# Kernel tuning notes

Hardware: AMD Instinct MI355X
Metric: run time of the kernel (lower is better)

## Reference

```python
import jax, jax.numpy as jnp
import numpy as np

DELTA_V = 0.5
DELTA_D = 1.5
LOSS_WEIGHT = 1.0


def setup_inputs() -> dict:
    key = jax.random.key(0)
    k1, k2, k3, k4 = jax.random.split(key, 4)
    B, D, H, W = 8, 4, 640, 640
    return {
        "emb": jax.random.normal(k1, (B, D, H, W), dtype=jnp.float32),
        "instance": jax.random.randint(k2, (B, H, W), 0, 33, dtype=jnp.int32),
        "kernel": jax.random.uniform(k3, (B, H, W), dtype=jnp.float32),
        "training_mask": jax.random.uniform(k4, (B, H, W), dtype=jnp.float32),
        "num_labels": 33,  # static: background label 0 + 32 instances, all present w.h.p.
    }


def _single(emb, instance, kernel, tmask, num_labels):
    # emb: [D,H,W]; instance: [H,W] int; kernel/tmask: [H,W] float
    D = emb.shape[0]
    tm = (tmask > 0.5).astype(instance.dtype)
    kn = (kernel > 0.5).astype(instance.dtype)
    inst2 = instance * tm                      # instance masked by training mask
    inst_k = (inst2 * kn).reshape(-1)          # kernel-restricted labels, [N]
    inst = inst2.reshape(-1)                   # [N]
    x = emb.reshape(D, -1).T                   # [N, D]
    ones = jnp.ones(x.shape[0], jnp.float32)

    # per-instance kernel means (scatter-mean), label 0 column forced to zero
    sums = jax.ops.segment_sum(x, inst_k, num_segments=num_labels)      # [K1, D]
    cnts = jax.ops.segment_sum(ones, inst_k, num_segments=num_labels)   # [K1]
    mean = sums / jnp.maximum(cnts, 1.0)[:, None]
    mean = mean.at[0].set(0.0)

    # aggregation term: per-pixel distance to its instance mean, segmented mean over labels 1..K
    diff = x - mean[inst]                                               # [N, D]
    dist = jnp.sqrt(jnp.sum(diff * diff, axis=1))
    val = jnp.log(jnp.maximum(dist - DELTA_V, 0.0) ** 2 + 1.0)
    cnt_i = jax.ops.segment_sum(ones, inst, num_segments=num_labels)
    agg = jax.ops.segment_sum(val, inst, num_segments=num_labels) / jnp.maximum(cnt_i, 1.0)
    l_agg = jnp.mean(agg[1:])

    # discrimination term: pairwise distances between instance means (exclude label 0 and diagonal)
    m = mean[1:]                                                        # [K, D]
    K = m.shape[0]
    pdiff = m[:, None, :] - m[None, :, :]
    pd = jnp.sqrt(jnp.sum(pdiff * pdiff, axis=-1) + jnp.eye(K))         # diag padded (masked below)
    vald = jnp.log(jnp.maximum(2.0 * DELTA_D - pd, 0.0) ** 2 + 1.0)
    off = 1.0 - jnp.eye(K)
    l_dis = jnp.sum(vald * off) / (K * (K - 1))

    # regularizer: mean over all num_labels columns; label-0 column contributes log(1)=0
    nrm1 = jnp.sqrt(jnp.sum(m * m, axis=1))
    l_reg = jnp.sum(jnp.log(nrm1 + 1.0)) / num_labels * 0.001

    return l_agg + l_dis + l_reg


def reference(emb, instance, kernel, training_mask, num_labels):
    f = lambda e, i, k, t: _single(e, i, k, t, num_labels)
    loss_batch = jax.vmap(f)(emb, instance, kernel, training_mask)
    return jnp.mean(LOSS_WEIGHT * loss_batch)
```

## Files before the change

### kernel.cpp

```cpp
#include <hip/hip_runtime.h>
#include <math.h>

#define HW    409600
#define HW4   102400
#define BATCH 8
#define NLAB  33
#define GXB1  100
#define NREP  8
#define RS    201
#define MEANS_OFF 0
#define AWS_OFF   1344
#define P2_OFF    3008
#define P1_OFF    4096
#define LABS_OFF_F 164096
#define NEED_SPLIT ((size_t)(P1_OFF + BATCH*GXB1*200) * 4)
#define NEED_LABS  ((size_t)LABS_OFF_F * 4 + (size_t)BATCH * HW4 * 4)

#if defined(__has_builtin) && __has_builtin(__builtin_amdgcn_sched_barrier)
#define SCHED_PIN() __builtin_amdgcn_sched_barrier(0)
#else
#define SCHED_PIN()
#endif

__global__ void init_ws(float* ws, float* out) {
    int t = threadIdx.x;
    for (int i = t; i < AWS_OFF + BATCH * 208 - 0; i += 256)
        if (i >= AWS_OFF) ws[i] = 0.f;
    if (t == 0) out[0] = 0.f;
}

__device__ __forceinline__ float getc(const float4& v, int e) {
    return (e == 0) ? v.x : (e == 1) ? v.y : (e == 2) ? v.z : v.w;
}
__device__ __forceinline__ float wave_sum(float v) {
    #pragma unroll
    for (int o = 32; o > 0; o >>= 1) v += __shfl_xor(v, o);
    return v;
}

struct Quad { int4 iv; float4 tv, kv, x0, x1, x2, x3; };

__device__ __forceinline__ void loadQ(Quad& q, const int4* inst4, const float4* tm4,
                                      const float4* kern4, const float4* emb4, int g) {
    q.iv = inst4[g];
    q.tv = tm4[g];
    q.kv = kern4[g];
    q.x0 = emb4[g];
    q.x1 = emb4[g + HW4];
    q.x2 = emb4[g + 2 * HW4];
    q.x3 = emb4[g + 3 * HW4];
}

__device__ __forceinline__ void acc1(int l, bool k,
                                     float x0, float x1, float x2, float x3,
                                     float* mb) {
    if (l) {
        float* bb = mb + l * 6;
        atomicAdd(bb + 5, 1.f);
        if (k) {
            atomicAdd(bb + 0, x0);
            atomicAdd(bb + 1, x1);
            atomicAdd(bb + 2, x2);
            atomicAdd(bb + 3, x3);
            atomicAdd(bb + 4, 1.f);
        }
    }
}

__device__ __forceinline__ void procQ(const Quad& q, float* mb,
                                      unsigned* labs, size_t labidx) {
    int l0 = (q.tv.x > 0.5f) ? q.iv.x : 0;
    int l1 = (q.tv.y > 0.5f) ? q.iv.y : 0;
    int l2 = (q.tv.z > 0.5f) ? q.iv.z : 0;
    int l3 = (q.tv.w > 0.5f) ? q.iv.w : 0;
    if (labs)
        labs[labidx] = (unsigned)l0 | ((unsigned)l1 << 8) |
                       ((unsigned)l2 << 16) | ((unsigned)l3 << 24);
    acc1(l0, q.kv.x > 0.5f, q.x0.x, q.x1.x, q.x2.x, q.x3.x, mb);
    acc1(l1, q.kv.y > 0.5f, q.x0.y, q.x1.y, q.x2.y, q.x3.y, mb);
    acc1(l2, q.kv.z > 0.5f, q.x0.z, q.x1.z, q.x2.z, q.x3.z, mb);
    acc1(l3, q.kv.w > 0.5f, q.x0.w, q.x1.w, q.x2.w, q.x3.w, mb);
}

template<bool SPLIT>
__global__ __launch_bounds__(256, 4) void pass1(const float* __restrict__ emb,
                                                const int*   __restrict__ inst,
                                                const float* __restrict__ kern,
                                                const float* __restrict__ tmask,
                                                float*       __restrict__ ws,
                                                unsigned*    __restrict__ labs) {
    __shared__ float bins[NREP][RS];
    const int t = threadIdx.x, bx = blockIdx.x, b = blockIdx.y;
    float* mb = bins[(t >> 3) & (NREP - 1)];

    const size_t  base  = (size_t)b * HW;
    const float4* emb4  = (const float4*)(emb + base * 4);
    const int4*   inst4 = (const int4*)(inst + base);
    const float4* kern4 = (const float4*)(kern + base);
    const float4* tm4   = (const float4*)(tmask + base);
    const int q0 = bx * 1024 + t;
    const size_t lb = (size_t)b * HW4;

    Quad c0, c1;
    loadQ(c0, inst4, tm4, kern4, emb4, q0);
    loadQ(c1, inst4, tm4, kern4, emb4, q0 + 256);
    SCHED_PIN();

    for (int i = t; i < NREP * RS; i += 256) (&bins[0][0])[i] = 0.f;
    __syncthreads();

    procQ(c0, mb, labs, lb + q0);
    loadQ(c0, inst4, tm4, kern4, emb4, q0 + 512);
    SCHED_PIN();
    procQ(c1, mb, labs, lb + q0 + 256);
    loadQ(c1, inst4, tm4, kern4, emb4, q0 + 768);
    SCHED_PIN();
    procQ(c0, mb, labs, lb + q0 + 512);
    procQ(c1, mb, labs, lb + q0 + 768);
    __syncthreads();

    if (t < NLAB * 6) {
        float v = 0.f;
        #pragma unroll
        for (int r = 0; r < NREP; ++r) v += bins[r][t];
        if (SPLIT) {
            ws[P1_OFF + ((size_t)b * GXB1 + bx) * 200 + t] = v;
        } else {
            if (v != 0.f) atomicAdd(ws + AWS_OFF + b * 208 + t, v);
        }
    }
}

template<bool SPLIT>
__global__ __launch_bounds__(256) void reduce_means(float* __restrict__ ws) {
    __shared__ float raw[200];
    const int t = threadIdx.x, b = blockIdx.x;
    if (t < NLAB * 6) {
        float s = 0.f;
        if (SPLIT) {
            const float* p = ws + P1_OFF + (size_t)b * GXB1 * 200;
            for (int bx = 0; bx < GXB1; ++bx) s += p[bx * 200 + t];
        } else {
            s = ws[AWS_OFF + b * 208 + t];
        }
        raw[t] = s;
    }
    __syncthreads();
    float* mm = ws + MEANS_OFF + b * 168;
    if (t < NLAB) {
        float cntk = raw[t * 6 + 4], cnti = raw[t * 6 + 5];
        float inv = 1.f / fmaxf(cntk, 1.f);
        float z = (t == 0) ? 0.f : 1.f;
        mm[t * 4 + 0] = z * raw[t * 6 + 0] * inv;
        mm[t * 4 + 1] = z * raw[t * 6 + 1] * inv;
        mm[t * 4 + 2] = z * raw[t * 6 + 2] * inv;
        mm[t * 4 + 3] = z * raw[t * 6 + 3] * inv;
        mm[132 + t]   = 1.f / fmaxf(cnti, 1.f);
    }
}

struct Quad2 { unsigned pk; int4 iv; float4 tv, x0, x1, x2, x3; };

template<bool USE_LABS>
__device__ __forceinline__ void loadQ2(Quad2& q, const unsigned* labs, size_t lb,
                                       const int4* inst4, const float4* tm4,
                                       const float4* emb4, int g) {
    if (USE_LABS) {
        q.pk = labs[lb + g];
    } else {
        q.iv = inst4[g];
        q.tv = tm4[g];
    }
    q.x0 = emb4[g];
    q.x1 = emb4[g + HW4];
    q.x2 = emb4[g + 2 * HW4];
    q.x3 = emb4[g + 3 * HW4];
}

template<bool USE_LABS>
__device__ __forceinline__ float procQ2(const Quad2& q, const float4* means4,
                                        const float* invci) {
    unsigned pk;
    if (USE_LABS) {
        pk = q.pk;
    } else {
        pk = (unsigned)((q.tv.x > 0.5f) ? q.iv.x : 0)        |
             ((unsigned)((q.tv.y > 0.5f) ? q.iv.y : 0) << 8) |
             ((unsigned)((q.tv.z > 0.5f) ? q.iv.z : 0) << 16)|
             ((unsigned)((q.tv.w > 0.5f) ? q.iv.w : 0) << 24);
    }
    float acc = 0.f;
    #pragma unroll
    for (int e = 0; e < 4; ++e) {
        int l = (pk >> (8 * e)) & 255;
        if (l) {
            float4 m = means4[l];
            float d0 = getc(q.x0, e) - m.x, d1 = getc(q.x1, e) - m.y;
            float d2 = getc(q.x2, e) - m.z, d3 = getc(q.x3, e) - m.w;
            float dist = sqrtf(d0 * d0 + d1 * d1 + d2 * d2 + d3 * d3);
            float u = fmaxf(dist - 0.5f, 0.f);
            acc += __logf(u * u + 1.f) * invci[l];
        }
    }
    return acc;
}

template<bool USE_LABS>
__global__ __launch_bounds__(256, 4) void pass2(const float* __restrict__ emb,
                                                const int*   __restrict__ inst,
                                                const float* __restrict__ tmask,
                                                float*       __restrict__ ws,
                                                const unsigned* __restrict__ labs) {
    __shared__ float4 means4[NLAB];
    __shared__ float  invci[NLAB];
    __shared__ float  red[4];
    const int t = threadIdx.x, bx = blockIdx.x, b = blockIdx.y;

    const size_t  base  = (size_t)b * HW;
    const float4* emb4  = (const float4*)(emb + base * 4);
    const int4*   inst4 = (const int4*)(inst + base);
    const float4* tm4   = (const float4*)(tmask + base);
    const int q0 = bx * 1024 + t;
    const size_t lb = (size_t)b * HW4;

    Quad2 c0, c1;
    loadQ2<USE_LABS>(c0, labs, lb, inst4, tm4, emb4, q0);
    loadQ2<USE_LABS>(c1, labs, lb, inst4, tm4, emb4, q0 + 256);
    SCHED_PIN();

    const float* mm = ws + MEANS_OFF + b * 168;
    if (t < NLAB) {
        means4[t] = ((const float4*)mm)[t];
        invci[t]  = mm[132 + t];
    }
    __syncthreads();

    float acc = procQ2<USE_LABS>(c0, means4, invci);
    loadQ2<USE_LABS>(c0, labs, lb, inst4, tm4, emb4, q0 + 512);
    SCHED_PIN();
    acc += procQ2<USE_LABS>(c1, means4, invci);
    loadQ2<USE_LABS>(c1, labs, lb, inst4, tm4, emb4, q0 + 768);
    SCHED_PIN();
    acc += procQ2<USE_LABS>(c0, means4, invci);
    acc += procQ2<USE_LABS>(c1, means4, invci);

    acc = wave_sum(acc);
    if ((t & 63) == 0) red[t >> 6] = acc;
    __syncthreads();
    if (t == 0)
        ws[P2_OFF + b * 128 + bx] = red[0] + red[1] + red[2] + red[3];
}

__global__ __launch_bounds__(256) void final_kernel(const float* __restrict__ ws,
                                                    float* __restrict__ out) {
    __shared__ float4 means4[NLAB];
    __shared__ float  red[4];
    const int t = threadIdx.x, b = blockIdx.x;
    const float* mm = ws + MEANS_OFF + b * 168;
    if (t < NLAB) means4[t] = ((const float4*)mm)[t];
    __syncthreads();

    float part = (t < GXB1) ? ws[P2_OFF + b * 128 + t] * (1.f / 32.f) : 0.f;
    float disp = 0.f;
    for (int p = t; p < 1024; p += 256) {
        int i = p >> 5, j = p & 31;
        if (i != j) {
            float4 mi = means4[i + 1], mj = means4[j + 1];
            float d0 = mi.x - mj.x, d1 = mi.y - mj.y;
            float d2 = mi.z - mj.z, d3 = mi.w - mj.w;
            float pd = sqrtf(d0 * d0 + d1 * d1 + d2 * d2 + d3 * d3);
            float u = fmaxf(3.0f - pd, 0.f);
            disp += __logf(u * u + 1.f);
        }
    }
    disp *= 1.f / 992.f;
    float regp = 0.f;
    if (t >= 1 && t < NLAB) {
        float4 m = means4[t];
        float n2 = m.x * m.x + m.y * m.y + m.z * m.z + m.w * m.w;
        regp = __logf(sqrtf(n2) + 1.f) * (0.001f / 33.f);
    }

    float v = wave_sum(part + disp + regp);
    if ((t & 63) == 0) red[t >> 6] = v;
    __syncthreads();
    if (t == 0)
        atomicAdd(out, (red[0] + red[1] + red[2] + red[3]) * (1.f / BATCH));
}

extern "C" void kernel_launch(void* const* d_in, const int* in_sizes, int n_in,
                              void* d_out, int out_size, void* d_ws, size_t ws_size,
                              hipStream_t stream) {
    const float* emb   = (const float*)d_in[0];
    const int*   inst  = (const int*)  d_in[1];
    const float* kern  = (const float*)d_in[2];
    const float* tmask = (const float*)d_in[3];
    float* ws  = (float*)d_ws;
    float* out = (float*)d_out;

    const bool split    = ws_size >= NEED_SPLIT;
    const bool use_labs = ws_size >= NEED_LABS;
    unsigned* labs = use_labs ? (unsigned*)(ws + LABS_OFF_F) : nullptr;

    init_ws<<<1, 256, 0, stream>>>(ws, out);
    dim3 grid(GXB1, BATCH);
    if (split) pass1<true ><<<grid, 256, 0, stream>>>(emb, inst, kern, tmask, ws, labs);
    else       pass1<false><<<grid, 256, 0, stream>>>(emb, inst, kern, tmask, ws, labs);
    if (split) reduce_means<true ><<<BATCH, 256, 0, stream>>>(ws);
    else       reduce_means<false><<<BATCH, 256, 0, stream>>>(ws);
    if (use_labs) pass2<true ><<<grid, 256, 0, stream>>>(emb, inst, tmask, ws, labs);
    else          pass2<false><<<grid, 256, 0, stream>>>(emb, inst, tmask, ws, nullptr);
    final_kernel<<<BATCH, 256, 0, stream>>>(ws, out);
}
```

Baseline: 156.7 us.

## Double grid size, drop init kernel, single-block final reduction

Halves the work per block in pass1 and pass2 (512 quads instead of 1024, grid 200x8) and raises the occupancy hint to 8 blocks per CU. Removes the init launch when the split path is used, and makes final_kernel a single block that loops over the batch and writes the output directly instead of using an atomic. The aim is more parallelism across the GPU plus fewer launches and atomics. In exchange the per-block partials double, and each block has less load-ahead to hide latency.

```diff
diff --git a/kernel.cpp b/kernel.cpp
--- a/kernel.cpp
+++ b/kernel.cpp
@@ -5,15 +5,15 @@
 #define HW4   102400
 #define BATCH 8
 #define NLAB  33
-#define GXB1  100
+#define GXB   200
 #define NREP  8
 #define RS    201
 #define MEANS_OFF 0
-#define AWS_OFF   1344
-#define P2_OFF    3008
-#define P1_OFF    4096
-#define LABS_OFF_F 164096
-#define NEED_SPLIT ((size_t)(P1_OFF + BATCH*GXB1*200) * 4)
+#define P2_OFF    2048
+#define AWS_OFF   4096
+#define P1_OFF    8192
+#define LABS_OFF_F (P1_OFF + BATCH*GXB*200)
+#define NEED_SPLIT ((size_t)LABS_OFF_F * 4)
 #define NEED_LABS  ((size_t)LABS_OFF_F * 4 + (size_t)BATCH * HW4 * 4)
 
 #if defined(__has_builtin) && __has_builtin(__builtin_amdgcn_sched_barrier)
@@ -22,11 +22,9 @@
 #define SCHED_PIN()
 #endif
 
-__global__ void init_ws(float* ws, float* out) {
-    int t = threadIdx.x;
-    for (int i = t; i < AWS_OFF + BATCH * 208 - 0; i += 256)
-        if (i >= AWS_OFF) ws[i] = 0.f;
-    if (t == 0) out[0] = 0.f;
+__global__ void init_aws(float* ws) {
+    int i = blockIdx.x * 256 + threadIdx.x;
+    if (i < BATCH * 208) ws[AWS_OFF + i] = 0.f;
 }
 
 __device__ __forceinline__ float getc(const float4& v, int e) {
@@ -83,7 +81,7 @@
 }
 
 template<bool SPLIT>
-__global__ __launch_bounds__(256, 4) void pass1(const float* __restrict__ emb,
+__global__ __launch_bounds__(256, 8) void pass1(const float* __restrict__ emb,
                                                 const int*   __restrict__ inst,
                                                 const float* __restrict__ kern,
                                                 const float* __restrict__ tmask,
@@ -98,25 +96,19 @@
     const int4*   inst4 = (const int4*)(inst + base);
     const float4* kern4 = (const float4*)(kern + base);
     const float4* tm4   = (const float4*)(tmask + base);
-    const int q0 = bx * 1024 + t;
+    const int q0 = bx * 512 + t;
     const size_t lb = (size_t)b * HW4;
 
-    Quad c0, c1;
-    loadQ(c0, inst4, tm4, kern4, emb4, q0);
-    loadQ(c1, inst4, tm4, kern4, emb4, q0 + 256);
+    for (int i = t; i < NREP * RS; i += 256) (&bins[0][0])[i] = 0.f;
+    __syncthreads();
+
+    Quad q;
+    loadQ(q, inst4, tm4, kern4, emb4, q0);
     SCHED_PIN();
-
-    for (int i = t; i < NREP * RS; i += 256) (&bins[0][0])[i] = 0.f;
-    __syncthreads();
-
-    procQ(c0, mb, labs, lb + q0);
-    loadQ(c0, inst4, tm4, kern4, emb4, q0 + 512);
+    procQ(q, mb, labs, lb + q0);
+    loadQ(q, inst4, tm4, kern4, emb4, q0 + 256);
     SCHED_PIN();
-    procQ(c1, mb, labs, lb + q0 + 256);
-    loadQ(c1, inst4, tm4, kern4, emb4, q0 + 768);
-    SCHED_PIN();
-    procQ(c0, mb, labs, lb + q0 + 512);
-    procQ(c1, mb, labs, lb + q0 + 768);
+    procQ(q, mb, labs, lb + q0 + 256);
     __syncthreads();
 
     if (t < NLAB * 6) {
@@ -124,7 +116,7 @@
         #pragma unroll
         for (int r = 0; r < NREP; ++r) v += bins[r][t];
         if (SPLIT) {
-            ws[P1_OFF + ((size_t)b * GXB1 + bx) * 200 + t] = v;
+            ws[P1_OFF + ((size_t)b * GXB + bx) * 200 + t] = v;
         } else {
             if (v != 0.f) atomicAdd(ws + AWS_OFF + b * 208 + t, v);
         }
@@ -138,8 +130,15 @@
     if (t < NLAB * 6) {
         float s = 0.f;
         if (SPLIT) {
-            const float* p = ws + P1_OFF + (size_t)b * GXB1 * 200;
-            for (int bx = 0; bx < GXB1; ++bx) s += p[bx * 200 + t];
+            const float* p = ws + P1_OFF + (size_t)b * GXB * 200 + t;
+            float s0 = 0.f, s1 = 0.f, s2 = 0.f, s3 = 0.f;
+            for (int bx = 0; bx < GXB; bx += 4) {
+                s0 += p[(bx + 0) * 200];
+                s1 += p[(bx + 1) * 200];
+                s2 += p[(bx + 2) * 200];
+                s3 += p[(bx + 3) * 200];
+            }
+            s = (s0 + s1) + (s2 + s3);
         } else {
             s = ws[AWS_OFF + b * 208 + t];
         }
@@ -206,7 +205,7 @@
 }
 
 template<bool USE_LABS>
-__global__ __launch_bounds__(256, 4) void pass2(const float* __restrict__ emb,
+__global__ __launch_bounds__(256, 8) void pass2(const float* __restrict__ emb,
                                                 const int*   __restrict__ inst,
                                                 const float* __restrict__ tmask,
                                                 float*       __restrict__ ws,
@@ -220,12 +219,11 @@
     const float4* emb4  = (const float4*)(emb + base * 4);
     const int4*   inst4 = (const int4*)(inst + base);
     const float4* tm4   = (const float4*)(tmask + base);
-    const int q0 = bx * 1024 + t;
+    const int q0 = bx * 512 + t;
     const size_t lb = (size_t)b * HW4;
 
-    Quad2 c0, c1;
-    loadQ2<USE_LABS>(c0, labs, lb, inst4, tm4, emb4, q0);
-    loadQ2<USE_LABS>(c1, labs, lb, inst4, tm4, emb4, q0 + 256);
+    Quad2 q;
+    loadQ2<USE_LABS>(q, labs, lb, inst4, tm4, emb4, q0);
     SCHED_PIN();
 
     const float* mm = ws + MEANS_OFF + b * 168;
@@ -235,57 +233,56 @@
     }
     __syncthreads();
 
-    float acc = procQ2<USE_LABS>(c0, means4, invci);
-    loadQ2<USE_LABS>(c0, labs, lb, inst4, tm4, emb4, q0 + 512);
+    float acc = procQ2<USE_LABS>(q, means4, invci);
+    loadQ2<USE_LABS>(q, labs, lb, inst4, tm4, emb4, q0 + 256);
     SCHED_PIN();
-    acc += procQ2<USE_LABS>(c1, means4, invci);
-    loadQ2<USE_LABS>(c1, labs, lb, inst4, tm4, emb4, q0 + 768);
-    SCHED_PIN();
-    acc += procQ2<USE_LABS>(c0, means4, invci);
-    acc += procQ2<USE_LABS>(c1, means4, invci);
+    acc += procQ2<USE_LABS>(q, means4, invci);
 
     acc = wave_sum(acc);
     if ((t & 63) == 0) red[t >> 6] = acc;
     __syncthreads();
     if (t == 0)
-        ws[P2_OFF + b * 128 + bx] = red[0] + red[1] + red[2] + red[3];
+        ws[P2_OFF + b * 256 + bx] = red[0] + red[1] + red[2] + red[3];
 }
 
 __global__ __launch_bounds__(256) void final_kernel(const float* __restrict__ ws,
                                                     float* __restrict__ out) {
     __shared__ float4 means4[NLAB];
     __shared__ float  red[4];
-    const int t = threadIdx.x, b = blockIdx.x;
-    const float* mm = ws + MEANS_OFF + b * 168;
-    if (t < NLAB) means4[t] = ((const float4*)mm)[t];
-    __syncthreads();
-
-    float part = (t < GXB1) ? ws[P2_OFF + b * 128 + t] * (1.f / 32.f) : 0.f;
-    float disp = 0.f;
-    for (int p = t; p < 1024; p += 256) {
-        int i = p >> 5, j = p & 31;
-        if (i != j) {
-            float4 mi = means4[i + 1], mj = means4[j + 1];
-            float d0 = mi.x - mj.x, d1 = mi.y - mj.y;
-            float d2 = mi.z - mj.z, d3 = mi.w - mj.w;
-            float pd = sqrtf(d0 * d0 + d1 * d1 + d2 * d2 + d3 * d3);
-            float u = fmaxf(3.0f - pd, 0.f);
-            disp += __logf(u * u + 1.f);
-        }
-    }
-    disp *= 1.f / 992.f;
-    float regp = 0.f;
-    if (t >= 1 && t < NLAB) {
-        float4 m = means4[t];
-        float n2 = m.x * m.x + m.y * m.y + m.z * m.z + m.w * m.w;
-        regp = __logf(sqrtf(n2) + 1.f) * (0.001f / 33.f);
-    }
-
-    float v = wave_sum(part + disp + regp);
-    if ((t & 63) == 0) red[t >> 6] = v;
-    __syncthreads();
-    if (t == 0)
-        atomicAdd(out, (red[0] + red[1] + red[2] + red[3]) * (1.f / BATCH));
+    const int t = threadIdx.x;
+    float total = 0.f;
+    for (int b = 0; b < BATCH; ++b) {
+        __syncthreads();
+        const float* mm = ws + MEANS_OFF + b * 168;
+        if (t < NLAB) means4[t] = ((const float4*)mm)[t];
+        __syncthreads();
+
+        float part = (t < GXB) ? ws[P2_OFF + b * 256 + t] * (1.f / 32.f) : 0.f;
+        float disp = 0.f;
+        for (int p = t; p < 1024; p += 256) {
+            int i = p >> 5, j = p & 31;
+            if (i != j) {
+                float4 mi = means4[i + 1], mj = means4[j + 1];
+                float d0 = mi.x - mj.x, d1 = mi.y - mj.y;
+                float d2 = mi.z - mj.z, d3 = mi.w - mj.w;
+                float pd = sqrtf(d0 * d0 + d1 * d1 + d2 * d2 + d3 * d3);
+                float u = fmaxf(3.0f - pd, 0.f);
+                disp += __logf(u * u + 1.f);
+            }
+        }
+        disp *= 1.f / 992.f;
+        float regp = 0.f;
+        if (t >= 1 && t < NLAB) {
+            float4 m = means4[t];
+            float n2 = m.x * m.x + m.y * m.y + m.z * m.z + m.w * m.w;
+            regp = __logf(sqrtf(n2) + 1.f) * (0.001f / 33.f);
+        }
+        float v = wave_sum(part + disp + regp);
+        if ((t & 63) == 0) red[t >> 6] = v;
+        __syncthreads();
+        if (t == 0) total += red[0] + red[1] + red[2] + red[3];
+    }
+    if (t == 0) out[0] = total * (1.f / BATCH);
 }
 
 extern "C" void kernel_launch(void* const* d_in, const int* in_sizes, int n_in,
@@ -302,13 +299,13 @@
     const bool use_labs = ws_size >= NEED_LABS;
     unsigned* labs = use_labs ? (unsigned*)(ws + LABS_OFF_F) : nullptr;
 
-    init_ws<<<1, 256, 0, stream>>>(ws, out);
-    dim3 grid(GXB1, BATCH);
+    if (!split) init_aws<<<dim3((BATCH * 208 + 255) / 256), 256, 0, stream>>>(ws);
+    dim3 grid(GXB, BATCH);
     if (split) pass1<true ><<<grid, 256, 0, stream>>>(emb, inst, kern, tmask, ws, labs);
     else       pass1<false><<<grid, 256, 0, stream>>>(emb, inst, kern, tmask, ws, labs);
     if (split) reduce_means<true ><<<BATCH, 256, 0, stream>>>(ws);
     else       reduce_means<false><<<BATCH, 256, 0, stream>>>(ws);
     if (use_labs) pass2<true ><<<grid, 256, 0, stream>>>(emb, inst, tmask, ws, labs);
     else          pass2<false><<<grid, 256, 0, stream>>>(emb, inst, tmask, ws, nullptr);
-    final_kernel<<<BATCH, 256, 0, stream>>>(ws, out);
-}
+    final_kernel<<<1, 256, 0, stream>>>(ws, out);
+}
```

After: 162.4 us. +3.7%, slower.
